# Performance work log

Hardware: AMD Instinct MI355X
Metric: run time of the kernel (lower is better)

## Reference

```python
import jax, jax.numpy as jnp
import numpy as np

B, T, D = 2, 2048, 2048
N, K, H = 8, 4, 256
WINDOW = 1024
BASE_FREQ = 10000
ROPE_PROP = 1.0
SCALE_FACTOR = 1.0
K_MASK = -2.3819763e+38


def apply_rope(inputs, positions, base_frequency, scale_factor=1.0, rope_proportion=1.0):
    # inputs: [B,L,N,H], positions: [B,L]
    head_dim = inputs.shape[-1]
    rope_angles = int(rope_proportion * head_dim // 2)
    nope_angles = head_dim // 2 - rope_angles
    freq_exponents = 2.0 / head_dim * jnp.arange(rope_angles, dtype=jnp.float32)
    timescale = jnp.pad(base_frequency ** freq_exponents, (0, nope_angles),
                        mode='constant', constant_values=(0, jnp.inf))
    sinusoid = positions[..., None].astype(jnp.float32) / timescale[None, None, :]
    sinusoid = sinusoid[..., None, :] / scale_factor  # [B,L,1,H//2]
    sin = jnp.sin(sinusoid)
    cos = jnp.cos(sinusoid)
    first, second = jnp.split(inputs, 2, axis=-1)
    out = jnp.concatenate([first * cos - second * sin,
                           second * cos + first * sin], axis=-1)
    return out.astype(inputs.dtype)


def rms_norm(x, scale, eps=1e-6):
    var = jnp.mean(jnp.square(x.astype(jnp.float32)), axis=-1, keepdims=True)
    normed = x * jax.lax.rsqrt(var + eps)
    return (normed * (1.0 + scale)).astype(x.dtype)


def setup_inputs() -> dict:
    key = jax.random.key(0)
    ks = jax.random.split(key, 5)
    std = 0.02
    return {
        'x': jax.random.normal(ks[0], (B, T, D), jnp.float32),
        'positions': jnp.broadcast_to(jnp.arange(T, dtype=jnp.int32), (B, T)),
        'q_w': jax.random.normal(ks[1], (N, D, H), jnp.float32) * std,
        'k_w': jax.random.normal(ks[2], (K, D, H), jnp.float32) * std,
        'v_w': jax.random.normal(ks[3], (K, D, H), jnp.float32) * std,
        'o_w': jax.random.normal(ks[4], (N, H, D), jnp.float32) * std,
        'q_norm_scale': jnp.zeros((H,), jnp.float32),
        'k_norm_scale': jnp.zeros((H,), jnp.float32),
    }


def reference(x, positions, q_w, k_w, v_w, o_w, q_norm_scale, k_norm_scale):
    # QKV projections (Einsum modules)
    q = jnp.einsum('btd,ndh->btnh', x, q_w)   # [B,T,N,H]
    k = jnp.einsum('bsd,kdh->bskh', x, k_w)   # [B,S,K,H]
    v = jnp.einsum('bsd,kdh->bskh', x, v_w)
    # QK RMSNorm (gemma-style, zero-centered scale)
    q = rms_norm(q, q_norm_scale)
    k = rms_norm(k, k_norm_scale)
    # RoPE (local attention: base 10000, full proportion)
    q = apply_rope(q, positions, BASE_FREQ, SCALE_FACTOR, ROPE_PROP)
    k = apply_rope(k, positions, BASE_FREQ, SCALE_FACTOR, ROPE_PROP)
    q = q * (H ** -0.5)
    # GQA: group queries over kv heads
    G = N // K
    qg = q.reshape(B, T, K, G, H)
    logits = jnp.einsum('btkgh,bskh->btkgs', qg, k)  # [B,T,K,G,S]
    # causal + sliding-window mask from positions
    qp = positions[:, :, None]
    kp = positions[:, None, :]
    mask = (kp <= qp) & (kp > qp - WINDOW)           # [B,T,S]
    logits = jnp.where(mask[:, :, None, None, :], logits, K_MASK)
    probs = jax.nn.softmax(logits.astype(jnp.float32), axis=-1).astype(logits.dtype)
    out = jnp.einsum('btkgs,bskh->btkgh', probs, v).reshape(B, T, N, H)
    return jnp.einsum('btnh,nhd->btd', out, o_w)
```

## Files before the change

kernel.cpp:

```cpp
#include <hip/hip_runtime.h>
#include <cmath>

#define T_SEQ 2048
#define WINDOW 1024

typedef __attribute__((ext_vector_type(8))) short bf16x8;
typedef __attribute__((ext_vector_type(4))) float f32x4;
typedef __attribute__((ext_vector_type(16))) float f32x16;

__device__ __forceinline__ unsigned short f2bf(float f) {
  union { float f; unsigned int u; } v; v.f = f;
  unsigned int r = v.u + 0x7FFFu + ((v.u >> 16) & 1u);
  return (unsigned short)(r >> 16);
}
__device__ __forceinline__ float bf2f(unsigned short u) {
  union { unsigned int i; float f; } v; v.i = ((unsigned int)u) << 16;
  return v.f;
}

#define GLD16(gp, lp)                                                  \
  __builtin_amdgcn_global_load_lds(                                    \
      (__attribute__((address_space(1))) unsigned int*)(gp),           \
      (__attribute__((address_space(3))) unsigned int*)(lp), 16, 0, 0)

__global__ __launch_bounds__(256) void cast_bf16(const float* __restrict__ in,
                                                 unsigned short* __restrict__ out) {
  size_t i = (size_t)blockIdx.x * 256 + threadIdx.x;
  float4 v = *(const float4*)&in[i * 4];
  ushort4 o;
  o.x = f2bf(v.x); o.y = f2bf(v.y); o.z = f2bf(v.z); o.w = f2bf(v.w);
  *(ushort4*)&out[i * 4] = o;
}

__global__ __launch_bounds__(256) void transpose_wqkv(
    const float* __restrict__ qw, const float* __restrict__ kw,
    const float* __restrict__ vw, unsigned short* __restrict__ bt) {
  __shared__ float tile[64][65];
  int c0 = blockIdx.x * 64;
  int d0 = blockIdx.y * 64;
  const float* src; int hbase;
  if (c0 < 2048) { src = qw + (size_t)(c0 >> 8) * 524288; hbase = c0 & 255; }
  else if (c0 < 3072) { int cc = c0 - 2048; src = kw + (size_t)(cc >> 8) * 524288; hbase = cc & 255; }
  else { int cc = c0 - 3072; src = vw + (size_t)(cc >> 8) * 524288; hbase = cc & 255; }
  int tx = threadIdx.x & 15, ty = threadIdx.x >> 4;
#pragma unroll
  for (int p = 0; p < 4; ++p) {
    float4 v = *(const float4*)&src[(size_t)(d0 + ty + 16 * p) * 256 + hbase + tx * 4];
    tile[ty + 16 * p][tx * 4 + 0] = v.x; tile[ty + 16 * p][tx * 4 + 1] = v.y;
    tile[ty + 16 * p][tx * 4 + 2] = v.z; tile[ty + 16 * p][tx * 4 + 3] = v.w;
  }
  __syncthreads();
#pragma unroll
  for (int p = 0; p < 4; ++p) {
    int hh = ty + 16 * p;
    ushort4 o;
    o.x = f2bf(tile[tx * 4 + 0][hh]); o.y = f2bf(tile[tx * 4 + 1][hh]);
    o.z = f2bf(tile[tx * 4 + 2][hh]); o.w = f2bf(tile[tx * 4 + 3][hh]);
    *(ushort4*)&bt[(size_t)(c0 + hh) * 2048 + d0 + tx * 4] = o;
  }
}

__global__ __launch_bounds__(256) void transpose_wo(
    const float* __restrict__ ow, unsigned short* __restrict__ wot) {
  __shared__ float tile[64][65];
  int j0 = blockIdx.x * 64;
  int d0 = blockIdx.y * 64;
  int tx = threadIdx.x & 15, ty = threadIdx.x >> 4;
#pragma unroll
  for (int p = 0; p < 4; ++p) {
    float4 v = *(const float4*)&ow[(size_t)(j0 + ty + 16 * p) * 2048 + d0 + tx * 4];
    tile[ty + 16 * p][tx * 4 + 0] = v.x; tile[ty + 16 * p][tx * 4 + 1] = v.y;
    tile[ty + 16 * p][tx * 4 + 2] = v.z; tile[ty + 16 * p][tx * 4 + 3] = v.w;
  }
  __syncthreads();
#pragma unroll
  for (int p = 0; p < 4; ++p) {
    int hh = ty + 16 * p;
    ushort4 o;
    o.x = f2bf(tile[tx * 4 + 0][hh]); o.y = f2bf(tile[tx * 4 + 1][hh]);
    o.z = f2bf(tile[tx * 4 + 2][hh]); o.w = f2bf(tile[tx * 4 + 3][hh]);
    *(ushort4*)&wot[(size_t)(d0 + hh) * 2048 + j0 + tx * 4] = o;
  }
}

__device__ __forceinline__ void gemm128_core(
    const unsigned short* __restrict__ A, const unsigned short* __restrict__ Bt,
    unsigned short* As, unsigned short* Bs, int m0, int n0, int K,
    f32x4 acc[4][4]) {
  const int tid = threadIdx.x;
  const int wave = tid >> 6, lane = tid & 63;
  const int wm = (wave & 1) << 6, wn = (wave >> 1) << 6;
  const int i0 = wave * 2, i1 = wave * 2 + 1;
  const int sr = lane >> 2;
  const int sc = (lane & 3) * 8;
  const size_t ar0 = (size_t)(m0 + i0 * 16 + sr) * K + sc;
  const size_t ar1 = (size_t)(m0 + i1 * 16 + sr) * K + sc;
  const size_t br0 = (size_t)(n0 + i0 * 16 + sr) * K + sc;
  const size_t br1 = (size_t)(n0 + i1 * 16 + sr) * K + sc;
  const int fm = lane & 15, fk = (lane >> 4) * 8;

  for (int kt = 0; kt < K; kt += 32) {
    GLD16(A + ar0 + kt, As + i0 * 512);
    GLD16(A + ar1 + kt, As + i1 * 512);
    GLD16(Bt + br0 + kt, Bs + i0 * 512);
    GLD16(Bt + br1 + kt, Bs + i1 * 512);
    __syncthreads();
    bf16x8 af[4], bv[4];
#pragma unroll
    for (int i = 0; i < 4; ++i)
      af[i] = *(const bf16x8*)&As[(wm + i * 16 + fm) * 32 + fk];
#pragma unroll
    for (int j = 0; j < 4; ++j)
      bv[j] = *(const bf16x8*)&Bs[(wn + j * 16 + fm) * 32 + fk];
#pragma unroll
    for (int i = 0; i < 4; ++i)
#pragma unroll
      for (int j = 0; j < 4; ++j)
        acc[i][j] = __builtin_amdgcn_mfma_f32_16x16x32_bf16(af[i], bv[j], acc[i][j], 0, 0, 0);
    __syncthreads();
  }
}

__global__ __launch_bounds__(256) void gemm_qkv_bf16(
    const unsigned short* __restrict__ xb, const unsigned short* __restrict__ wt,
    unsigned short* __restrict__ qo, unsigned short* __restrict__ ko,
    unsigned short* __restrict__ vo) {
  __shared__ unsigned short As[128 * 32];
  __shared__ unsigned short Bs[128 * 32];
  const int n0 = blockIdx.x * 128, m0 = blockIdx.y * 128;
  f32x4 acc[4][4];
#pragma unroll
  for (int i = 0; i < 4; ++i)
#pragma unroll
    for (int j = 0; j < 4; ++j) acc[i][j] = {0.f, 0.f, 0.f, 0.f};
  gemm128_core(xb, wt, As, Bs, m0, n0, 2048, acc);

  unsigned short* obase; int ldo, cb;
  if (n0 < 2048) { obase = qo; ldo = 2048; cb = n0; }
  else if (n0 < 3072) { obase = ko; ldo = 1024; cb = n0 - 2048; }
  else { obase = vo; ldo = 1024; cb = n0 - 3072; }
  const int lane = threadIdx.x & 63, wave = threadIdx.x >> 6;
  const int wm = (wave & 1) << 6, wn = (wave >> 1) << 6;
  const int rbase = m0 + wm + (lane >> 4) * 4;
  const int cbase = cb + wn + (lane & 15);
#pragma unroll
  for (int i = 0; i < 4; ++i)
#pragma unroll
    for (int j = 0; j < 4; ++j)
#pragma unroll
      for (int r = 0; r < 4; ++r)
        obase[(size_t)(rbase + i * 16 + r) * ldo + cbase + j * 16] = f2bf(acc[i][j][r]);
}

__global__ __launch_bounds__(256) void gemm_out_bf16(
    const unsigned short* __restrict__ ab, const unsigned short* __restrict__ wot,
    float* __restrict__ out) {
  __shared__ unsigned short As[128 * 32];
  __shared__ unsigned short Bs[128 * 32];
  const int n0 = blockIdx.x * 128, m0 = blockIdx.y * 128;
  f32x4 acc[4][4];
#pragma unroll
  for (int i = 0; i < 4; ++i)
#pragma unroll
    for (int j = 0; j < 4; ++j) acc[i][j] = {0.f, 0.f, 0.f, 0.f};
  gemm128_core(ab, wot, As, Bs, m0, n0, 2048, acc);

  const int lane = threadIdx.x & 63, wave = threadIdx.x >> 6;
  const int wm = (wave & 1) << 6, wn = (wave >> 1) << 6;
  const int rbase = m0 + wm + (lane >> 4) * 4;
  const int cbase = n0 + wn + (lane & 15);
#pragma unroll
  for (int i = 0; i < 4; ++i)
#pragma unroll
    for (int j = 0; j < 4; ++j)
#pragma unroll
      for (int r = 0; r < 4; ++r)
        out[(size_t)(rbase + i * 16 + r) * 2048 + cbase + j * 16] = acc[i][j][r];
}

__global__ __launch_bounds__(64) void rope_norm_bf16(
    unsigned short* __restrict__ qb, unsigned short* __restrict__ kb,
    const int* __restrict__ positions,
    const float* __restrict__ qns, const float* __restrict__ kns) {
  int row = blockIdx.x;
  int lane = threadIdx.x;
  unsigned short* ptr; const float* ns; float extra; int bt;
  if (row < 32768) {
    ptr = qb + (size_t)row * 256; ns = qns; extra = 0.0625f; bt = row >> 3;
  } else {
    int r = row - 32768;
    ptr = kb + (size_t)r * 256; ns = kns; extra = 1.0f; bt = r >> 2;
  }
  int pos = positions[bt];

  ushort4 u = *(const ushort4*)&ptr[lane << 2];
  float xv[4] = {bf2f(u.x), bf2f(u.y), bf2f(u.z), bf2f(u.w)};
  float ss = xv[0]*xv[0] + xv[1]*xv[1] + xv[2]*xv[2] + xv[3]*xv[3];
#pragma unroll
  for (int off = 1; off < 64; off <<= 1) ss += __shfl_xor(ss, off, 64);
  float rinv = rsqrtf(ss * (1.0f / 256.0f) + 1e-6f);

  float4 sc4 = *(const float4*)&ns[lane << 2];
  xv[0] *= rinv * (1.0f + sc4.x);
  xv[1] *= rinv * (1.0f + sc4.y);
  xv[2] *= rinv * (1.0f + sc4.z);
  xv[3] *= rinv * (1.0f + sc4.w);

  float ov[4];
#pragma unroll
  for (int c = 0; c < 4; ++c) ov[c] = __shfl_xor(xv[c], 32, 64);

  int hr = (lane & 31) << 2;
  float sgn = (lane < 32) ? -1.0f : 1.0f;
  ushort4 w;
  unsigned short res[4];
#pragma unroll
  for (int c = 0; c < 4; ++c) {
    float invts = exp2f(-(float)(hr + c) * 0.10381025296523007f);
    float angle = (float)pos * invts;
    float sn, cs;
    sincosf(angle, &sn, &cs);
    res[c] = f2bf((xv[c] * cs + sgn * ov[c] * sn) * extra);
  }
  w.x = res[0]; w.y = res[1]; w.z = res[2]; w.w = res[3];
  *(ushort4*)&ptr[lane << 2] = w;
}

__global__ __launch_bounds__(256) void transpose_v(
    const unsigned short* __restrict__ vbf, unsigned short* __restrict__ vt) {
  __shared__ unsigned short tile[64][68];
  int h0 = blockIdx.x * 64;
  int t0 = blockIdx.y * 64;
  int z = blockIdx.z;
  int tx = threadIdx.x & 15, ty = threadIdx.x >> 4;
  const unsigned short* src = vbf + ((size_t)(z >> 2) * 8192 + (z & 3)) * 256;
#pragma unroll
  for (int p = 0; p < 4; ++p) {
    ushort4 v = *(const ushort4*)&src[(size_t)(t0 + ty + 16 * p) * 1024 + h0 + tx * 4];
    tile[ty + 16 * p][tx * 4 + 0] = v.x; tile[ty + 16 * p][tx * 4 + 1] = v.y;
    tile[ty + 16 * p][tx * 4 + 2] = v.z; tile[ty + 16 * p][tx * 4 + 3] = v.w;
  }
  __syncthreads();
  unsigned short* dst = vt + (size_t)z * 256 * 2048;
#pragma unroll
  for (int p = 0; p < 4; ++p) {
    int hh = ty + 16 * p;
    ushort4 o;
    o.x = tile[tx * 4 + 0][hh]; o.y = tile[tx * 4 + 1][hh];
    o.z = tile[tx * 4 + 2][hh]; o.w = tile[tx * 4 + 3][hh];
    *(ushort4*)&dst[(size_t)(h0 + hh) * 2048 + t0 + tx * 4] = o;
  }
}

__global__ __launch_bounds__(128, 1) void attn_mfma(
    const unsigned short* __restrict__ qb,
    const unsigned short* __restrict__ kb,
    const unsigned short* __restrict__ vt,
    unsigned short* __restrict__ ob) {
  __shared__ __align__(16) unsigned short Kl[8192];
  __shared__ __align__(16) unsigned short Vl[8192];
  __shared__ __align__(16) unsigned short Ps[2048];

  const int tid = threadIdx.x;
  const int w = tid >> 6, lane = tid & 63;
  const int l5 = lane >> 5, l31 = lane & 31;
  const int t0 = blockIdx.x * 64;
  const int n = blockIdx.y, b = blockIdx.z;
  const int kvh = n >> 1;
  const int tminw = t0 + 32 * w, tmaxw = tminw + 31;

  bf16x8 aq[16];
  {
    const unsigned short* qrow =
        qb + (((size_t)b * 2048 + tminw + l31) * 8 + n) * 256 + l5 * 8;
#pragma unroll
    for (int kc = 0; kc < 16; ++kc) aq[kc] = *(const bf16x8*)(qrow + kc * 16);
  }

  f32x16 O[8], lsum;
#pragma unroll
  for (int i = 0; i < 8; ++i)
#pragma unroll
    for (int r = 0; r < 16; ++r) O[i][r] = 0.f;
#pragma unroll
  for (int r = 0; r < 16; ++r) lsum[r] = 0.f;

  bf16x8 ones;
#pragma unroll
  for (int i = 0; i < 8; ++i) ones[i] = (short)0x3F80;

  const unsigned short* kbase = kb + ((size_t)b * 8192 + kvh) * 256;
  const unsigned short* vbase = vt + (size_t)(b * 4 + kvh) * 256 * 2048;

  int s_lo = t0 - 1024; if (s_lo < 0) s_lo = 0;

  for (int s0 = s_lo; s0 < t0 + 64; s0 += 32) {
    __syncthreads();
#pragma unroll
    for (int j = 0; j < 8; ++j) {
      int g = j * 128 + tid;
      int kc = g >> 6, s = (g >> 1) & 31, hi = g & 1;
      GLD16(kbase + (size_t)(s0 + s) * 1024 + kc * 16 + hi * 8,
            Kl + (j * 128 + w * 64) * 8);
    }
#pragma unroll
    for (int j = 0; j < 8; ++j) {
      int g = j * 128 + tid;
      int kc2 = g >> 9, h = (g >> 1) & 255, hi = g & 1;
      GLD16(vbase + (size_t)h * 2048 + s0 + kc2 * 16 + hi * 8,
            Vl + (j * 128 + w * 64) * 8);
    }
    __syncthreads();

    bool skip = (s0 > tmaxw) || (s0 + 31 < tminw - 1023);
    if (!skip) {
      f32x16 pa, pb;
#pragma unroll
      for (int r = 0; r < 16; ++r) { pa[r] = 0.f; pb[r] = 0.f; }
#pragma unroll
      for (int kc = 0; kc < 16; kc += 2) {
        bf16x8 b0 = *(const bf16x8*)&Kl[kc * 512 + l31 * 16 + l5 * 8];
        bf16x8 b1 = *(const bf16x8*)&Kl[(kc + 1) * 512 + l31 * 16 + l5 * 8];
        pa = __builtin_amdgcn_mfma_f32_32x32x16_bf16(aq[kc], b0, pa, 0, 0, 0);
        pb = __builtin_amdgcn_mfma_f32_32x32x16_bf16(aq[kc + 1], b1, pb, 0, 0, 0);
      }

      bool allvalid = (s0 + 31 <= tminw) && (s0 >= tmaxw - 1023);
      int scol = s0 + l31;
#pragma unroll
      for (int r = 0; r < 16; ++r) {
        float sv = pa[r] + pb[r];
        float p = exp2f(sv * 1.442695040888963f);
        int m = (r & 3) + 8 * (r >> 2) + 4 * l5;
        if (!allvalid) {
          int dt = (tminw + m) - scol;
          p = (dt >= 0 && dt < 1024) ? p : 0.f;
        }
        Ps[w * 1024 + (l31 >> 4) * 512 + m * 16 + (l31 & 15)] = f2bf(p);
      }

      bf16x8 pf0 = *(const bf16x8*)&Ps[w * 1024 + l31 * 16 + l5 * 8];
      bf16x8 pf1 = *(const bf16x8*)&Ps[w * 1024 + 512 + l31 * 16 + l5 * 8];
      lsum = __builtin_amdgcn_mfma_f32_32x32x16_bf16(pf0, ones, lsum, 0, 0, 0);
      lsum = __builtin_amdgcn_mfma_f32_32x32x16_bf16(pf1, ones, lsum, 0, 0, 0);
#pragma unroll
      for (int hb = 0; hb < 8; ++hb) {
        bf16x8 v0 = *(const bf16x8*)&Vl[(hb * 32 + l31) * 16 + l5 * 8];
        bf16x8 v1 = *(const bf16x8*)&Vl[4096 + (hb * 32 + l31) * 16 + l5 * 8];
        O[hb] = __builtin_amdgcn_mfma_f32_32x32x16_bf16(pf0, v0, O[hb], 0, 0, 0);
        O[hb] = __builtin_amdgcn_mfma_f32_32x32x16_bf16(pf1, v1, O[hb], 0, 0, 0);
      }
    }
  }

  unsigned short* obase = ob + (((size_t)b * 2048 + tminw) * 8 + n) * 256;
#pragma unroll
  for (int r = 0; r < 16; ++r) {
    int m = (r & 3) + 8 * (r >> 2) + 4 * l5;
    float rinv = 1.0f / lsum[r];
    size_t rowoff = (size_t)m * 2048;
#pragma unroll
    for (int hb = 0; hb < 8; ++hb)
      obase[rowoff + hb * 32 + l31] = f2bf(O[hb][r] * rinv);
  }
}

extern "C" void kernel_launch(void* const* d_in, const int* in_sizes, int n_in,
                              void* d_out, int out_size, void* d_ws, size_t ws_size,
                              hipStream_t stream) {
  const float* x   = (const float*)d_in[0];
  const int* pos   = (const int*)d_in[1];
  const float* q_w = (const float*)d_in[2];
  const float* k_w = (const float*)d_in[3];
  const float* v_w = (const float*)d_in[4];
  const float* o_w = (const float*)d_in[5];
  const float* qns = (const float*)d_in[6];
  const float* kns = (const float*)d_in[7];
  float* out = (float*)d_out;

  unsigned short* W = (unsigned short*)d_ws;
  unsigned short* qb0   = W;
  unsigned short* kb0   = W + 8388608;
  unsigned short* vbf   = W + 12582912;
  unsigned short* vtb   = W + 16777216;
  unsigned short* xb    = W + 20971520;
  unsigned short* wqkvt = W + 29360128;
  unsigned short* abuf  = wqkvt;
  unsigned short* wot   = W + 37748736;

  cast_bf16<<<dim3(8192), 256, 0, stream>>>(x, xb);
  transpose_wqkv<<<dim3(64, 32), 256, 0, stream>>>(q_w, k_w, v_w, wqkvt);
  gemm_qkv_bf16<<<dim3(32, 32), 256, 0, stream>>>(xb, wqkvt, qb0, kb0, vbf);
  transpose_wo<<<dim3(32, 32), 256, 0, stream>>>(o_w, wot);
  rope_norm_bf16<<<dim3(49152), 64, 0, stream>>>(qb0, kb0, pos, qns, kns);
  transpose_v<<<dim3(4, 32, 8), 256, 0, stream>>>(vbf, vtb);
  attn_mfma<<<dim3(32, 8, 2), 128, 0, stream>>>(qb0, kb0, vtb, abuf);
  gemm_out_bf16<<<dim3(16, 32), 256, 0, stream>>>(abuf, wot, out);
}
```

Baseline: 395.8 us.

## Share KV tiles across GQA head pair and double-buffer K/V staging

The attention kernel now uses 256-thread blocks, one per KV head, so the two query heads of a GQA group share a single staged K/V tile. This halves the global-to-LDS traffic per query head. K/V staging is double-buffered: the next tile's global_load_lds copies are issued right after the barrier, so they can overlap the MFMA work on the current tile, and there is one barrier per iteration instead of two. RoPE switches from sincosf to the fast __sincosf intrinsic, which trades some angle accuracy at large positions for fewer instructions. LDS use roughly doubles, and correctness depends on the async copies having completed before the barrier.

```diff
diff --git a/kernel.cpp b/kernel.cpp
--- a/kernel.cpp
+++ b/kernel.cpp
@@ -219,7 +219,7 @@
     float invts = exp2f(-(float)(hr + c) * 0.10381025296523007f);
     float angle = (float)pos * invts;
     float sn, cs;
-    sincosf(angle, &sn, &cs);
+    __sincosf(angle, &sn, &cs);
     res[c] = f2bf((xv[c] * cs + sgn * ov[c] * sn) * extra);
   }
   w.x = res[0]; w.y = res[1]; w.z = res[2]; w.w = res[3];
@@ -252,22 +252,22 @@
   }
 }
 
-__global__ __launch_bounds__(128, 1) void attn_mfma(
+__global__ __launch_bounds__(256, 1) void attn_mfma(
     const unsigned short* __restrict__ qb,
     const unsigned short* __restrict__ kb,
     const unsigned short* __restrict__ vt,
     unsigned short* __restrict__ ob) {
-  __shared__ __align__(16) unsigned short Kl[8192];
-  __shared__ __align__(16) unsigned short Vl[8192];
-  __shared__ __align__(16) unsigned short Ps[2048];
+  __shared__ __align__(16) unsigned short Kl[16384];
+  __shared__ __align__(16) unsigned short Vl[16384];
+  __shared__ __align__(16) unsigned short Ps[4096];
 
   const int tid = threadIdx.x;
   const int w = tid >> 6, lane = tid & 63;
   const int l5 = lane >> 5, l31 = lane & 31;
   const int t0 = blockIdx.x * 64;
-  const int n = blockIdx.y, b = blockIdx.z;
-  const int kvh = n >> 1;
-  const int tminw = t0 + 32 * w, tmaxw = tminw + 31;
+  const int kvh = blockIdx.y, b = blockIdx.z;
+  const int n = 2 * kvh + (w >> 1);
+  const int tminw = t0 + 32 * (w & 1), tmaxw = tminw + 31;
 
   bf16x8 aq[16];
   {
@@ -293,34 +293,43 @@
   const unsigned short* vbase = vt + (size_t)(b * 4 + kvh) * 256 * 2048;
 
   int s_lo = t0 - 1024; if (s_lo < 0) s_lo = 0;
-
-  for (int s0 = s_lo; s0 < t0 + 64; s0 += 32) {
+  const int s_end = t0 + 64;
+
+#define STAGE(buf, s0)                                                        \
+  {                                                                           \
+    _Pragma("unroll") for (int j = 0; j < 4; ++j) {                           \
+      int g = j * 256 + tid;                                                  \
+      int kc = g >> 6, s = (g >> 1) & 31, hi = g & 1;                         \
+      GLD16(kbase + (size_t)((s0) + s) * 1024 + kc * 16 + hi * 8,             \
+            Kl + (buf) * 8192 + (j * 256 + w * 64) * 8);                      \
+    }                                                                         \
+    _Pragma("unroll") for (int j = 0; j < 4; ++j) {                           \
+      int g = j * 256 + tid;                                                  \
+      int kc2 = g >> 9, h = (g >> 1) & 255, hi = g & 1;                       \
+      GLD16(vbase + (size_t)h * 2048 + (s0) + kc2 * 16 + hi * 8,              \
+            Vl + (buf) * 8192 + (j * 256 + w * 64) * 8);                      \
+    }                                                                         \
+  }
+
+  STAGE(0, s_lo);
+  int buf = 0;
+
+  for (int s0 = s_lo; s0 < s_end; s0 += 32, buf ^= 1) {
     __syncthreads();
-#pragma unroll
-    for (int j = 0; j < 8; ++j) {
-      int g = j * 128 + tid;
-      int kc = g >> 6, s = (g >> 1) & 31, hi = g & 1;
-      GLD16(kbase + (size_t)(s0 + s) * 1024 + kc * 16 + hi * 8,
-            Kl + (j * 128 + w * 64) * 8);
-    }
-#pragma unroll
-    for (int j = 0; j < 8; ++j) {
-      int g = j * 128 + tid;
-      int kc2 = g >> 9, h = (g >> 1) & 255, hi = g & 1;
-      GLD16(vbase + (size_t)h * 2048 + s0 + kc2 * 16 + hi * 8,
-            Vl + (j * 128 + w * 64) * 8);
-    }
-    __syncthreads();
+    int s1 = s0 + 32;
+    if (s1 < s_end) STAGE(buf ^ 1, s1);
 
     bool skip = (s0 > tmaxw) || (s0 + 31 < tminw - 1023);
     if (!skip) {
+      const unsigned short* Kb = Kl + buf * 8192;
+      const unsigned short* Vb = Vl + buf * 8192;
       f32x16 pa, pb;
 #pragma unroll
       for (int r = 0; r < 16; ++r) { pa[r] = 0.f; pb[r] = 0.f; }
 #pragma unroll
       for (int kc = 0; kc < 16; kc += 2) {
-        bf16x8 b0 = *(const bf16x8*)&Kl[kc * 512 + l31 * 16 + l5 * 8];
-        bf16x8 b1 = *(const bf16x8*)&Kl[(kc + 1) * 512 + l31 * 16 + l5 * 8];
+        bf16x8 b0 = *(const bf16x8*)&Kb[kc * 512 + l31 * 16 + l5 * 8];
+        bf16x8 b1 = *(const bf16x8*)&Kb[(kc + 1) * 512 + l31 * 16 + l5 * 8];
         pa = __builtin_amdgcn_mfma_f32_32x32x16_bf16(aq[kc], b0, pa, 0, 0, 0);
         pb = __builtin_amdgcn_mfma_f32_32x32x16_bf16(aq[kc + 1], b1, pb, 0, 0, 0);
       }
@@ -345,8 +354,8 @@
       lsum = __builtin_amdgcn_mfma_f32_32x32x16_bf16(pf1, ones, lsum, 0, 0, 0);
 #pragma unroll
       for (int hb = 0; hb < 8; ++hb) {
-        bf16x8 v0 = *(const bf16x8*)&Vl[(hb * 32 + l31) * 16 + l5 * 8];
-        bf16x8 v1 = *(const bf16x8*)&Vl[4096 + (hb * 32 + l31) * 16 + l5 * 8];
+        bf16x8 v0 = *(const bf16x8*)&Vb[(hb * 32 + l31) * 16 + l5 * 8];
+        bf16x8 v1 = *(const bf16x8*)&Vb[4096 + (hb * 32 + l31) * 16 + l5 * 8];
         O[hb] = __builtin_amdgcn_mfma_f32_32x32x16_bf16(pf0, v0, O[hb], 0, 0, 0);
         O[hb] = __builtin_amdgcn_mfma_f32_32x32x16_bf16(pf1, v1, O[hb], 0, 0, 0);
       }
@@ -394,6 +403,6 @@
   transpose_wo<<<dim3(32, 32), 256, 0, stream>>>(o_w, wot);
   rope_norm_bf16<<<dim3(49152), 64, 0, stream>>>(qb0, kb0, pos, qns, kns);
   transpose_v<<<dim3(4, 32, 8), 256, 0, stream>>>(vbf, vtb);
-  attn_mfma<<<dim3(32, 8, 2), 128, 0, stream>>>(qb0, kb0, vtb, abuf);
+  attn_mfma<<<dim3(32, 4, 2), 256, 0, stream>>>(qb0, kb0, vtb, abuf);
   gemm_out_bf16<<<dim3(16, 32), 256, 0, stream>>>(abuf, wot, out);
 }
```

Measured after the change: 393.8 us. About the same (-0.5%).
